# Performance work log

Hardware: AMD Instinct MI355X
Metric: run time of the kernel (lower is better)

Reference implementation:

```python
import jax, jax.numpy as jnp
import numpy as np
from jax import lax

DN3D = ('NDHWC', 'DHWIO', 'NDHWC')


def _conv3d(x, w):
    return lax.conv_general_dilated(x, w, window_strides=(1, 1, 1),
                                    padding='VALID', dimension_numbers=DN3D)


def _cconv3d(xr, xi, wr, wi):
    # (xr + i xi) * (wr + i wi)
    yr = _conv3d(xr, wr) - _conv3d(xi, wi)
    yi = _conv3d(xr, wi) + _conv3d(xi, wr)
    return yr, yi


def _project(wr, wi, zero_mean):
    # zero-mean + bound-norm weight projection over (kD,kH,kW,Cin) per output filter
    ax = (0, 1, 2, 3)
    if zero_mean:
        wr = wr - jnp.mean(wr, ax, keepdims=True)
        wi = wi - jnp.mean(wi, ax, keepdims=True)
    norm = jnp.sqrt(jnp.sum(wr * wr + wi * wi, ax, keepdims=True))
    s = 1.0 / jnp.maximum(norm, 1.0)
    return wr * s, wi * s


def _sympad(x, pads):
    # pads: list of (lo, hi) per axis
    return jnp.pad(x, pads, mode='symmetric')


def setup_inputs() -> dict:
    key = jax.random.key(0)
    ks = jax.random.split(key, 6)
    B, T, Z, Y, X, C = 2, 8, 20, 64, 64, 2
    F1, F = 32, 32
    return {
        'xr': jax.random.normal(ks[0], (B, T, Z, Y, X, C), jnp.float32),
        'xi': jax.random.normal(ks[1], (B, T, Z, Y, X, C), jnp.float32),
        'wxyz_r': jax.random.normal(ks[2], (3, 3, 3, C, F1), jnp.float32) * 0.1,
        'wxyz_i': jax.random.normal(ks[3], (3, 3, 3, C, F1), jnp.float32) * 0.1,
        'wt_r': jax.random.normal(ks[4], (3, 1, 1, F1, F), jnp.float32) * 0.1,
        'wt_i': jax.random.normal(ks[5], (3, 1, 1, F1, F), jnp.float32) * 0.1,
    }


def reference(xr, xi, wxyz_r, wxyz_i, wt_r, wt_i):
    B, T, Z, Y, X, C = xr.shape
    kz, ky, kx = wxyz_r.shape[0], wxyz_r.shape[1], wxyz_r.shape[2]
    kt = wt_r.shape[0]
    F1 = wxyz_r.shape[-1]
    F = wt_r.shape[-1]

    # projected (zero-mean, bound-norm) complex kernels
    wsr, wsi = _project(wxyz_r, wxyz_i, zero_mean=True)
    wtr, wti = _project(wt_r, wt_i, zero_mean=False)

    # --- spatial 3D conv over (Z,Y,X): fold T into batch (== per-T-slice loop)
    sr = xr.reshape(B * T, Z, Y, X, C)
    si = xi.reshape(B * T, Z, Y, X, C)
    pads_sp = [(0, 0), (kz // 2, kz // 2), (ky // 2, ky // 2), (kx // 2, kx // 2), (0, 0)]
    sr = _sympad(sr, pads_sp)
    si = _sympad(si, pads_sp)
    spr, spi = _cconv3d(sr, si, wsr, wsi)          # [B*T, Z, Y, X, F1]
    spr = spr.reshape(B, T, Z, Y, X, F1)
    spi = spi.reshape(B, T, Z, Y, X, F1)

    # --- temporal conv (kt,1,1) over (T,Z,Y): fold X into batch (== per-X-slice loop)
    tr = spr.transpose(0, 4, 1, 2, 3, 5).reshape(B * X, T, Z, Y, F1)
    ti = spi.transpose(0, 4, 1, 2, 3, 5).reshape(B * X, T, Z, Y, F1)
    pads_t = [(0, 0), (kt // 2, kt // 2), (0, 0), (0, 0), (0, 0)]
    tr = _sympad(tr, pads_t)
    ti = _sympad(ti, pads_t)
    ytr, yti = _cconv3d(tr, ti, wtr, wti)          # [B*X, T, Z, Y, F]
    yr = ytr.reshape(B, X, T, Z, Y, F).transpose(0, 2, 3, 4, 1, 5)
    yi = yti.reshape(B, X, T, Z, Y, F).transpose(0, 2, 3, 4, 1, 5)
    return yr, yi
```

## Files before the change

kernel.cpp:

```cpp
#include <hip/hip_runtime.h>

#define B_ 2
#define T_ 8
#define Z_ 20
#define Y_ 64
#define X_ 64
#define C_ 2
#define F1_ 32
#define F_ 32

constexpr int NPTS = B_*T_*Z_*Y_*X_;
constexpr int ZYX  = Z_*Y_*X_;

constexpr int RING_STRIDE = 36;
constexpr int SLOT_DW     = 16*RING_STRIDE;

using bf8   = __attribute__((ext_vector_type(8))) short;
using f32x4 = __attribute__((ext_vector_type(4))) float;

__device__ inline unsigned short f2bf(float x) {
    unsigned u = __builtin_bit_cast(unsigned, x);
    return (unsigned short)((u + 0x7fff + ((u >> 16) & 1)) >> 16);
}
__device__ inline unsigned pk(float a, float b) {
    return (unsigned)f2bf(a) | ((unsigned)f2bf(b) << 16);
}

__global__ __launch_bounds__(64) void project_kernel(
    const float* __restrict__ wxr, const float* __restrict__ wxi,
    const float* __restrict__ wtr, const float* __restrict__ wti,
    float* __restrict__ psr, float* __restrict__ psi,
    float* __restrict__ otr, float* __restrict__ oti)
{
    const int bid  = blockIdx.x;
    const int lane = threadIdx.x;

    if (bid < F1_) {
        const int f = bid;
        float er = 0.f, ei = 0.f;
        if (lane < 54) { er = wxr[lane*F1_ + f]; ei = wxi[lane*F1_ + f]; }
        float sr = er, si = ei;
        #pragma unroll
        for (int o = 32; o >= 1; o >>= 1) { sr += __shfl_xor(sr, o); si += __shfl_xor(si, o); }
        const float mr = sr * (1.f/54.f), mi = si * (1.f/54.f);
        const float dr = er - mr, di = ei - mi;
        float sq = (lane < 54) ? (dr*dr + di*di) : 0.f;
        #pragma unroll
        for (int o = 32; o >= 1; o >>= 1) sq += __shfl_xor(sq, o);
        const float s = 1.f / fmaxf(sqrtf(sq), 1.f);
        if (lane < 54) { psr[lane*F1_ + f] = dr*s; psi[lane*F1_ + f] = di*s; }
    } else {
        const int f = bid - F1_;
        float er[2], ei[2];
        float sq = 0.f;
        #pragma unroll
        for (int k = 0; k < 2; ++k) {
            const int e = lane + k*64;
            if (e < 96) { er[k] = wtr[e*F_ + f]; ei[k] = wti[e*F_ + f]; sq += er[k]*er[k] + ei[k]*ei[k]; }
            else        { er[k] = 0.f;  ei[k] = 0.f; }
        }
        #pragma unroll
        for (int o = 32; o >= 1; o >>= 1) sq += __shfl_xor(sq, o);
        const float s = 1.f / fmaxf(sqrtf(sq), 1.f);
        #pragma unroll
        for (int k = 0; k < 2; ++k) {
            const int e = lane + k*64;
            if (e < 96) { otr[e*F_ + f] = er[k]*s; oti[e*F_ + f] = ei[k]*s; }
        }
    }
}

__global__ __launch_bounds__(256) void pack_kernel(
    const float* __restrict__ psr, const float* __restrict__ psi,
    const float* __restrict__ ptr_, const float* __restrict__ pti,
    unsigned short* __restrict__ wsp, unsigned short* __restrict__ wp)
{
    const int g = blockIdx.x;
    if (g < 16) {
        for (int o = g*512 + threadIdx.x; o < (g+1)*512; o += 256) {
            const int j  = o & 7;
            const int l  = (o >> 3) & 63;
            const int gg = o >> 9;
            const int kb = gg & 3, ct = gg >> 2;
            const int k  = kb*32 + (l >> 4)*8 + j;
            const int n  = ct*16 + (l & 15);
            float v = 0.f;
            if (k < 108) {
                const int tap = k >> 2, q = k & 3, cin = q & 1, cp = q >> 1;
                const int f  = n & 31;
                const float wr = psr[(tap*2 + cin)*F1_ + f];
                const float wi = psi[(tap*2 + cin)*F1_ + f];
                v = (n < 32) ? (cp ? -wi : wr) : (cp ? wr : wi);
            }
            wsp[o] = f2bf(v);
        }
    } else {
        for (int o = (g-16)*512 + threadIdx.x; o < (g-15)*512; o += 256) {
            const int j  = o & 7;
            const int l  = (o >> 3) & 63;
            const int gg = o >> 9;
            const int kb = gg % 6, ct = gg / 6;
            const int k  = kb*32 + (l >> 4)*8 + j;
            const int n  = ct*16 + (l & 15);
            const int kt = k >> 6, f1 = (k >> 1) & 31, c = k & 1;
            const int f  = n & 31;
            const float wr = ptr_[(kt*F1_ + f1)*F_ + f];
            const float wi = pti[(kt*F1_ + f1)*F_ + f];
            const float v  = (n < 32) ? (c ? -wi : wr) : (c ? wr : wi);
            wp[o] = f2bf(v);
        }
    }
}

__global__ __launch_bounds__(256) void repack_kernel(
    const float* __restrict__ xr, const float* __restrict__ xi,
    uint2* __restrict__ xb)
{
    const int p = blockIdx.x*256 + threadIdx.x;
    const float2 vr = *reinterpret_cast<const float2*>(xr + (size_t)p*2);
    const float2 vi = *reinterpret_cast<const float2*>(xi + (size_t)p*2);
    uint2 v;
    v.x = (unsigned)f2bf(vr.x) | ((unsigned)f2bf(vr.y) << 16);
    v.y = (unsigned)f2bf(vi.x) | ((unsigned)f2bf(vi.y) << 16);
    xb[p] = v;
}

__global__ __launch_bounds__(256) void fused_kernel(
    const uint2* __restrict__ xb,
    const unsigned short* __restrict__ wsp,
    const unsigned short* __restrict__ wp,
    float* __restrict__ yr, float* __restrict__ yi)
{
    __shared__ uint4 ring4[4*3*SLOT_DW/4];
    unsigned* ring = reinterpret_cast<unsigned*>(ring4);

    const int tid  = threadIdx.x;
    const int lane = tid & 63;
    const int wid  = tid >> 6;
    const int lx   = lane & 15;
    const int lg   = lane >> 4;

    const int bq = blockIdx.x;
    const int y  = bq & 63;
    const int z  = (bq >> 6) % Z_;
    const int b  = bq / (64*Z_);
    const int x0 = wid * 16;

    bf8 wsf[4][4];
    const bf8* w8 = reinterpret_cast<const bf8*>(wsp);
    #pragma unroll
    for (int ct = 0; ct < 4; ++ct)
        #pragma unroll
        for (int kb = 0; kb < 4; ++kb)
            wsf[ct][kb] = w8[(ct*4 + kb)*64 + lane];

    bf8 wtf[4][6];
    const bf8* wp8 = reinterpret_cast<const bf8*>(wp);
    #pragma unroll
    for (int ct = 0; ct < 4; ++ct)
        #pragma unroll
        for (int kb = 0; kb < 6; ++kb)
            wtf[ct][kb] = wp8[(ct*6 + kb)*64 + lane];

    int off[4][2];
    #pragma unroll
    for (int kb = 0; kb < 4; ++kb)
        #pragma unroll
        for (int s = 0; s < 2; ++s) {
            int ta = kb*8 + lg*2 + s; if (ta > 26) ta = 26;
            const int dz = ta/9, dyx = ta - dz*9, dy = dyx/3, dx = dyx - dy*3;
            int zz = z + dz - 1;      zz = zz < 0 ? 0 : (zz >= Z_ ? Z_-1 : zz);
            int yy = y + dy - 1;      yy = yy < 0 ? 0 : (yy >= Y_ ? Y_-1 : yy);
            int xx = x0 + lx + dx - 1; xx = xx < 0 ? 0 : (xx >= X_ ? X_-1 : xx);
            off[kb][s] = (zz*Y_ + yy)*X_ + xx;
        }

    unsigned* myring  = ring + wid*3*SLOT_DW;
    const int  rbase  = lx*RING_STRIDE + lg*4;
    const size_t orow = (((size_t)b*T_)*Z_ + z)*(size_t)(Y_*X_) + (size_t)y*X_ + x0 + lx;

    uint4 cur_lo, cur_hi;

    auto SPATIAL = [&](int t) {
        const uint2* xt = xb + (size_t)(b*T_ + t)*ZYX;
        bf8 af[4];
        #pragma unroll
        for (int kb = 0; kb < 4; ++kb) {
            const uint2 l2 = xt[off[kb][0]];
            const uint2 h2 = xt[off[kb][1]];
            af[kb] = __builtin_bit_cast(bf8, make_uint4(l2.x, l2.y, h2.x, h2.y));
        }
        f32x4 acc[4];
        #pragma unroll
        for (int ct = 0; ct < 4; ++ct) acc[ct] = (f32x4){0.f,0.f,0.f,0.f};
        #pragma unroll
        for (int ct = 0; ct < 4; ++ct)
            #pragma unroll
            for (int kb = 0; kb < 4; ++kb)
                acc[ct] = __builtin_amdgcn_mfma_f32_16x16x32_bf16(
                              wsf[ct][kb], af[kb], acc[ct], 0, 0, 0);
        cur_lo = make_uint4(pk(acc[0][0],acc[2][0]), pk(acc[0][1],acc[2][1]),
                            pk(acc[0][2],acc[2][2]), pk(acc[0][3],acc[2][3]));
        cur_hi = make_uint4(pk(acc[1][0],acc[3][0]), pk(acc[1][1],acc[3][1]),
                            pk(acc[1][2],acc[3][2]), pk(acc[1][3],acc[3][3]));
    };

    auto WRITE = [&](int t) {
        unsigned* s = myring + (t % 3)*SLOT_DW + rbase;
        *reinterpret_cast<uint4*>(s)      = cur_lo;
        *reinterpret_cast<uint4*>(s + 16) = cur_hi;
    };

    auto EMIT = [&](int sa, int sb, int tout) {
        const unsigned* pa = myring + (sa % 3)*SLOT_DW + rbase;
        const unsigned* pb = myring + (sb % 3)*SLOT_DW + rbase;
        bf8 fr[6];
        fr[0] = __builtin_bit_cast(bf8, *reinterpret_cast<const uint4*>(pa));
        fr[1] = __builtin_bit_cast(bf8, *reinterpret_cast<const uint4*>(pa + 16));
        fr[2] = __builtin_bit_cast(bf8, *reinterpret_cast<const uint4*>(pb));
        fr[3] = __builtin_bit_cast(bf8, *reinterpret_cast<const uint4*>(pb + 16));
        fr[4] = __builtin_bit_cast(bf8, cur_lo);
        fr[5] = __builtin_bit_cast(bf8, cur_hi);
        f32x4 acc[4];
        #pragma unroll
        for (int ct = 0; ct < 4; ++ct) acc[ct] = (f32x4){0.f,0.f,0.f,0.f};
        #pragma unroll
        for (int ct = 0; ct < 4; ++ct)
            #pragma unroll
            for (int kb = 0; kb < 6; ++kb)
                acc[ct] = __builtin_amdgcn_mfma_f32_16x16x32_bf16(
                              wtf[ct][kb], fr[kb], acc[ct], 0, 0, 0);
        const size_t p = orow + (size_t)tout * ZYX;
        #pragma unroll
        for (int ct = 0; ct < 4; ++ct) {
            float* outp = (ct < 2) ? yr : yi;
            *reinterpret_cast<f32x4*>(outp + p*F_ + (ct & 1)*16 + lg*4) = acc[ct];
        }
    };

    SPATIAL(0);
    WRITE(0);
    #pragma unroll 1
    for (int t = 1; t < T_; ++t) {
        SPATIAL(t);
        EMIT(t-2 < 0 ? 0 : t-2, t-1, t-1);
        WRITE(t);
    }
    EMIT(T_-2, T_-1, T_-1);
}

extern "C" void kernel_launch(void* const* d_in, const int* in_sizes, int n_in,
                              void* d_out, int out_size, void* d_ws, size_t ws_size,
                              hipStream_t stream)
{
    const float* xr  = (const float*)d_in[0];
    const float* xi  = (const float*)d_in[1];
    const float* wxr = (const float*)d_in[2];
    const float* wxi = (const float*)d_in[3];
    const float* wtr = (const float*)d_in[4];
    const float* wti = (const float*)d_in[5];

    float* ws   = (float*)d_ws;
    float* psr  = ws;
    float* psi  = ws + 2048;
    float* ptr_ = ws + 4096;
    float* pti  = ws + 8192;
    unsigned short* wsp = (unsigned short*)(ws + 12288);
    unsigned short* wp  = (unsigned short*)(ws + 16384);
    uint2* xb           = (uint2*)(ws + 32768);

    float* yr = (float*)d_out;
    float* yi = yr + (size_t)NPTS * F_;

    hipLaunchKernelGGL(project_kernel, dim3(64), dim3(64), 0, stream,
                       wxr, wxi, wtr, wti, psr, psi, ptr_, pti);
    hipLaunchKernelGGL(pack_kernel, dim3(40), dim3(256), 0, stream,
                       psr, psi, ptr_, pti, wsp, wp);
    hipLaunchKernelGGL(repack_kernel, dim3(NPTS/256), dim3(256), 0, stream,
                       xr, xi, xb);
    hipLaunchKernelGGL(fused_kernel, dim3(B_*Z_*Y_), dim3(256), 0, stream,
                       xb, wsp, wp, yr, yi);
}
```

Before: 104.8 us.

## Stage spatial input halo in LDS with double-buffered prefetch

Each wave now loads a 3x3x18 halo slab of the packed input into shared memory once per time step, instead of gathering 8 overlapping global loads per lane. MFMA operands are then read from LDS. The next step's slab is fetched into registers while the current step computes, which hides global latency. Launch bounds now ask for 2 blocks per CU. This costs extra LDS and register pressure, and it relies on per-wave LDS visibility without an explicit barrier.

```diff
diff --git a/kernel.cpp b/kernel.cpp
--- a/kernel.cpp
+++ b/kernel.cpp
@@ -14,6 +14,7 @@
 
 constexpr int RING_STRIDE = 36;
 constexpr int SLOT_DW     = 16*RING_STRIDE;
+constexpr int HALO        = 3*3*18;
 
 using bf8   = __attribute__((ext_vector_type(8))) short;
 using f32x4 = __attribute__((ext_vector_type(4))) float;
@@ -125,13 +126,14 @@
     xb[p] = v;
 }
 
-__global__ __launch_bounds__(256) void fused_kernel(
+__global__ __launch_bounds__(256, 2) void fused_kernel(
     const uint2* __restrict__ xb,
     const unsigned short* __restrict__ wsp,
     const unsigned short* __restrict__ wp,
     float* __restrict__ yr, float* __restrict__ yi)
 {
     __shared__ uint4 ring4[4*3*SLOT_DW/4];
+    __shared__ uint2 slab[4][2][HALO];
     unsigned* ring = reinterpret_cast<unsigned*>(ring4);
 
     const int tid  = threadIdx.x;
@@ -162,17 +164,27 @@
         for (int kb = 0; kb < 6; ++kb)
             wtf[ct][kb] = wp8[(ct*6 + kb)*64 + lane];
 
-    int off[4][2];
+    int xoff[3];
+    #pragma unroll
+    for (int i = 0; i < 3; ++i) {
+        int it = lane + i*64; if (it >= HALO) it = HALO-1;
+        const int iz = it / 54;
+        const int iy = (it / 18) % 3;
+        const int ix = it % 18;
+        int zz = z + iz - 1;  zz = zz < 0 ? 0 : (zz >= Z_ ? Z_-1 : zz);
+        int yy = y + iy - 1;  yy = yy < 0 ? 0 : (yy >= Y_ ? Y_-1 : yy);
+        int xx = x0 + ix - 1; xx = xx < 0 ? 0 : (xx >= X_ ? X_-1 : xx);
+        xoff[i] = (zz*Y_ + yy)*X_ + xx;
+    }
+
+    int o8[4][2];
     #pragma unroll
     for (int kb = 0; kb < 4; ++kb)
         #pragma unroll
         for (int s = 0; s < 2; ++s) {
             int ta = kb*8 + lg*2 + s; if (ta > 26) ta = 26;
             const int dz = ta/9, dyx = ta - dz*9, dy = dyx/3, dx = dyx - dy*3;
-            int zz = z + dz - 1;      zz = zz < 0 ? 0 : (zz >= Z_ ? Z_-1 : zz);
-            int yy = y + dy - 1;      yy = yy < 0 ? 0 : (yy >= Y_ ? Y_-1 : yy);
-            int xx = x0 + lx + dx - 1; xx = xx < 0 ? 0 : (xx >= X_ ? X_-1 : xx);
-            off[kb][s] = (zz*Y_ + yy)*X_ + xx;
+            o8[kb][s] = (dz*3 + dy)*18 + dx + lx;
         }
 
     unsigned* myring  = ring + wid*3*SLOT_DW;
@@ -180,15 +192,29 @@
     const size_t orow = (((size_t)b*T_)*Z_ + z)*(size_t)(Y_*X_) + (size_t)y*X_ + x0 + lx;
 
     uint4 cur_lo, cur_hi;
-
-    auto SPATIAL = [&](int t) {
+    uint2 stmp[3];
+
+    auto STAGE_ISSUE = [&](int t) {
         const uint2* xt = xb + (size_t)(b*T_ + t)*ZYX;
+        stmp[0] = xt[xoff[0]];
+        stmp[1] = xt[xoff[1]];
+        if (lane < HALO - 128) stmp[2] = xt[xoff[2]];
+    };
+    auto STAGE_WRITE = [&](int bufsel) {
+        uint2* s = slab[wid][bufsel];
+        s[lane]      = stmp[0];
+        s[lane + 64] = stmp[1];
+        if (lane < HALO - 128) s[lane + 128] = stmp[2];
+    };
+
+    auto SPATIAL = [&](int bufsel) {
+        const uint2* s = slab[wid][bufsel];
         bf8 af[4];
         #pragma unroll
         for (int kb = 0; kb < 4; ++kb) {
-            const uint2 l2 = xt[off[kb][0]];
-            const uint2 h2 = xt[off[kb][1]];
-            af[kb] = __builtin_bit_cast(bf8, make_uint4(l2.x, l2.y, h2.x, h2.y));
+            const uint2 lo = s[o8[kb][0]];
+            const uint2 hi = s[o8[kb][1]];
+            af[kb] = __builtin_bit_cast(bf8, make_uint4(lo.x, lo.y, hi.x, hi.y));
         }
         f32x4 acc[4];
         #pragma unroll
@@ -238,11 +264,17 @@
         }
     };
 
+    STAGE_ISSUE(0);
+    STAGE_WRITE(0);
+    STAGE_ISSUE(1);
     SPATIAL(0);
     WRITE(0);
+
     #pragma unroll 1
     for (int t = 1; t < T_; ++t) {
-        SPATIAL(t);
+        STAGE_WRITE(t & 1);
+        if (t < T_-1) STAGE_ISSUE(t+1);
+        SPATIAL(t & 1);
         EMIT(t-2 < 0 ? 0 : t-2, t-1, t-1);
         WRITE(t);
     }
```

Result: faster. 97.54 us (-7.0%).
